# Optimization experiments

Measured on AMD Instinct MI355X. Metric: run time of the kernel, lower is better.

## Reference

```python
import jax, jax.numpy as jnp
import numpy as np

N_HEAD = 16

def setup_inputs() -> dict:
    key = jax.random.key(0)
    k1, k2, k3 = jax.random.split(key, 3)
    B, S, D = 2, 2048, 1024
    x = jax.random.normal(k1, (B, S, D), dtype=jnp.float32)
    w_attn = jax.random.normal(k2, (D, 3 * D), dtype=jnp.float32) * 0.02
    b_attn = jnp.zeros((3 * D,), dtype=jnp.float32)
    w_proj = jax.random.normal(k3, (D, D), dtype=jnp.float32) * 0.02
    b_proj = jnp.zeros((D,), dtype=jnp.float32)
    return {"x": x, "w_attn": w_attn, "b_attn": b_attn, "w_proj": w_proj, "b_proj": b_proj}

def reference(x, w_attn, b_attn, w_proj, b_proj):
    B, S, D = x.shape
    hd = D // N_HEAD
    qkv = x @ w_attn + b_attn                      # [B,S,3D]
    q, k, v = jnp.split(qkv, 3, axis=-1)
    def heads(t):  # [B,S,D] -> [B,H,S,hd]
        return t.reshape(B, S, N_HEAD, hd).transpose(0, 2, 1, 3)
    q, k, v = heads(q), heads(k), heads(v)
    # NOTE: original forward applies NO scaling and NO causal mask; dropout=eval (identity)
    scores = jnp.einsum('bhqd,bhkd->bhqk', q, k)   # [B,H,S,S]
    probs = jax.nn.softmax(scores, axis=-1)
    out = jnp.einsum('bhqk,bhkd->bhqd', probs, v)  # [B,H,S,hd]
    out = out.transpose(0, 2, 1, 3).reshape(B, S, D)
    return out @ w_proj + b_proj
```

## Files before the change

kernel.cpp:

```cpp
#include <hip/hip_runtime.h>

typedef _Float16 f16;
typedef _Float16 f16x8 __attribute__((ext_vector_type(8)));
typedef _Float16 f16x4 __attribute__((ext_vector_type(4)));
typedef float    f32x4 __attribute__((ext_vector_type(4)));
typedef unsigned int u32;
typedef unsigned int u32x4 __attribute__((ext_vector_type(4)));

#define LOG2E 1.44269504088896340736f
#define EXPC  (13.0f * 1.44269504088896340736f)

__device__ __forceinline__ void gload_lds16(const void* g, void* l) {
  __builtin_amdgcn_global_load_lds(
      (const __attribute__((address_space(1))) void*)g,
      (__attribute__((address_space(3))) void*)l, 16, 0, 0);
}

__device__ __forceinline__ void block_sync() {
  asm volatile("" ::: "memory");
  __builtin_amdgcn_s_barrier();
  asm volatile("" ::: "memory");
}

__global__ __launch_bounds__(256)
void k_prep(const float* __restrict__ x, f16* __restrict__ xh,
            const float* __restrict__ w_attn, f16* __restrict__ waT,
            const float* __restrict__ w_proj, f16* __restrict__ wpT) {
  __shared__ float tile[32][33];
  const int bid = blockIdx.x;
  const int t = threadIdx.x;
  if (bid < 4096) {
    int i = bid * 256 + t;
    f32x4 v = ((const f32x4*)x)[i];
    f16x4 o;
    o[0] = (f16)v[0]; o[1] = (f16)v[1]; o[2] = (f16)v[2]; o[3] = (f16)v[3];
    ((f16x4*)xh)[i] = o;
    return;
  }
  const float* in; f16* out; int R, C, bx, by;
  if (bid < 4096 + 3072) {
    int q = bid - 4096; in = w_attn; out = waT; R = 1024; C = 3072;
    bx = q % 96; by = q / 96;
  } else {
    int q = bid - 7168; in = w_proj; out = wpT; R = 1024; C = 1024;
    bx = q % 32; by = q / 32;
  }
  int tx = t & 31, ty = t >> 5;
  int c0 = bx * 32, r0 = by * 32;
#pragma unroll
  for (int i = 0; i < 4; i++)
    tile[ty + i * 8][tx] = in[(size_t)(r0 + ty + i * 8) * C + c0 + tx];
  __syncthreads();
#pragma unroll
  for (int i = 0; i < 4; i++)
    out[(size_t)(c0 + ty + i * 8) * R + r0 + tx] = (f16)tile[tx][ty + i * 8];
}

template <int EPI>
__global__ __launch_bounds__(256)
void k_gemm(const f16* __restrict__ A, const f16* __restrict__ BT,
            const float* __restrict__ bias,
            f16* __restrict__ out_qk, f16* __restrict__ out_vT,
            float* __restrict__ out_f) {
  constexpr int K = 1024;
  __shared__ f16 smem[4][128 * 64];
  const int t = threadIdx.x;
  const int l = t & 63;
  const int w = t >> 6;
  const int wm = (w >> 1) * 64;
  const int wn = (w & 1) * 64;
  const int m0 = blockIdx.x * 128;
  const int n0 = blockIdx.y * 128;
  const int lr = l & 15;
  const int lg = l >> 4;
  const int fr8 = lr & 7;

  const int row8g = t >> 3;
  const int scg = (t & 7) ^ (row8g & 7);
  const f16* Ap = A + (size_t)(m0 + row8g) * K + scg * 8;
  const f16* Bp = BT + (size_t)(n0 + row8g) * K + scg * 8;

#define GSTAGE(buf) do { \
    _Pragma("unroll") \
    for (int i2 = 0; i2 < 4; i2++) \
      gload_lds16(Ap + (size_t)(i2 * 32) * K, &smem[buf][(i2 * 256 + t) * 8]); \
    _Pragma("unroll") \
    for (int i2 = 0; i2 < 4; i2++) \
      gload_lds16(Bp + (size_t)(i2 * 32) * K, &smem[2 + buf][(i2 * 256 + t) * 8]); \
    Ap += 64; Bp += 64; } while (0)

  f32x4 acc[4][4] = {};

#define GCOMPUTE(buf) do { \
    _Pragma("unroll") \
    for (int kk = 0; kk < 64; kk += 32) { \
      const int cbase = (kk >> 3) + lg; \
      f16x8 af[4], bf[4]; \
      _Pragma("unroll") \
      for (int i = 0; i < 4; i++) \
        af[i] = *(const f16x8*)&smem[buf][((wm + i * 16 + lr) * 8 + (cbase ^ fr8)) * 8]; \
      _Pragma("unroll") \
      for (int j = 0; j < 4; j++) \
        bf[j] = *(const f16x8*)&smem[2 + buf][((wn + j * 16 + lr) * 8 + (cbase ^ fr8)) * 8]; \
      _Pragma("unroll") \
      for (int i = 0; i < 4; i++) \
        _Pragma("unroll") \
        for (int j = 0; j < 4; j++) \
          acc[i][j] = __builtin_amdgcn_mfma_f32_16x16x32_f16(af[i], bf[j], acc[i][j], 0, 0, 0); \
    } } while (0)

  GSTAGE(0);
  asm volatile("s_waitcnt vmcnt(0)" ::: "memory");
  block_sync();

  for (int kt = 0; kt < 16; kt += 2) {
    GSTAGE(1);
    GCOMPUTE(0);
    asm volatile("s_waitcnt vmcnt(0)" ::: "memory");
    block_sync();
    if (kt + 2 < 16) GSTAGE(0);
    GCOMPUTE(1);
    asm volatile("s_waitcnt vmcnt(0)" ::: "memory");
    block_sync();
  }
#undef GSTAGE
#undef GCOMPUTE

  if (EPI == 1) {
#pragma unroll
    for (int i = 0; i < 4; i++) {
      int mbase = m0 + wm + i * 16 + (l >> 4) * 4;
#pragma unroll
      for (int j = 0; j < 4; j++) {
        int n = n0 + wn + j * 16 + lr;
        float bv = bias[n];
#pragma unroll
        for (int r = 0; r < 4; r++)
          out_f[(size_t)(mbase + r) * 1024 + n] = acc[i][j][r] + bv;
      }
    }
  } else if (n0 < 2048) {
#pragma unroll
    for (int i = 0; i < 4; i++) {
      int mbase = m0 + wm + i * 16 + (l >> 4) * 4;
#pragma unroll
      for (int j = 0; j < 4; j++) {
        int n = n0 + wn + j * 16 + lr;
        float bv = bias[n];
        float sc = (n0 + wn + j * 16 < 1024) ? LOG2E : 1.0f;
#pragma unroll
        for (int r = 0; r < 4; r++)
          out_qk[(size_t)(mbase + r) * 2048 + n] = (f16)((acc[i][j][r] + bv) * sc);
      }
    }
  } else {
    f16* scr = &smem[0][0];
#pragma unroll
    for (int i = 0; i < 4; i++) {
      int s0 = wm + i * 16 + (l >> 4) * 4;
#pragma unroll
      for (int j = 0; j < 4; j++) {
        int nl = wn + j * 16 + lr;
        float bv = bias[n0 + nl];
        f16x4 pv;
#pragma unroll
        for (int r = 0; r < 4; r++) pv[r] = (f16)(acc[i][j][r] + bv);
        *(f16x4*)&scr[nl * 128 + (s0 ^ ((nl & 15) << 3))] = pv;
      }
    }
    block_sync();
    const int b = m0 >> 11;
    const int kvc0 = (m0 & 2047) >> 3;
    const int h0 = (n0 - 2048) >> 6;
    const int l64 = t & 63;
    const int wv = t >> 6;
#pragma unroll
    for (int p = 0; p < 8; p++) {
      int pair = wv + p * 4;
      int kvcl = pair & 15;
      int hgl  = pair >> 4;
      int nl = hgl * 64 + l64;
      f16x8 vv = *(const f16x8*)&scr[nl * 128 + ((kvcl * 8) ^ ((nl & 15) << 3))];
      size_t dst = (((size_t)(b * 16 + h0 + hgl) * 256 + kvc0 + kvcl) * 64 + l64) * 8;
      *(f16x8*)&out_vT[dst] = vv;
    }
  }
}

__global__ __launch_bounds__(256, 4)
void k_attn(const f16* __restrict__ qk, const f16* __restrict__ vT,
            f16* __restrict__ aout) {
  __shared__ f16 Kl[2][64 * 64];
  const int t = threadIdx.x;
  const int l = t & 63;
  const int w = t >> 6;
  const int lr = l & 15;
  const int lg = l >> 4;
  const int lk = lg * 8;
  const int r7x = lr & 7;

  const int o  = (blockIdx.x & 7) * 128 + (blockIdx.x >> 3);
  const int qt = o & 31;
  const int bh = o >> 5;
  const int b  = bh >> 4;
  const int h  = bh & 15;
  const int q0 = qt * 64 + w * 16;

  const f16* qp = qk + (size_t)(b * 2048 + q0 + lr) * 2048 + h * 64 + lk;
  f16x8 qf0 = *(const f16x8*)qp;
  f16x8 qf1 = *(const f16x8*)(qp + 32);

  const f16* kg = qk + (size_t)(b * 2048) * 2048 + 1024 + h * 64;
  const int r5 = t >> 3;
  const int u_s = r5 & 15;
  const int prow = (u_s >> 2) * 8 + (u_s & 3) * 2 + (r5 >> 4);
  const int sc_s = ((t & 7) ^ (r5 & 7)) << 3;

  const f16* vg0 = vT + (((size_t)bh * 256 + lg) * 64 + lr) * 8;

#define STAGE(B) do { \
    gload_lds16(kg + (size_t)(prow     ) * 2048 + sc_s, &Kl[B][(      t) * 8]); \
    gload_lds16(kg + (size_t)(prow + 32) * 2048 + sc_s, &Kl[B][(256 + t) * 8]); \
    kg += 64 * 2048; } while (0)

  f32x4 oa[4] = {};
  f32x4 ssum = {};
  const f32x4 initc = {-EXPC, -EXPC, -EXPC, -EXPC};
  f16x8 ones;
#pragma unroll
  for (int j = 0; j < 8; j++) ones[j] = (f16)1.0f;

  STAGE(0);
  asm volatile("s_waitcnt vmcnt(0)" ::: "memory");
  block_sync();

#define TILE_BODY(B) do { \
    f16x8 vfr[4][2]; \
    _Pragma("unroll") \
    for (int c4 = 0; c4 < 4; c4++) \
      _Pragma("unroll") \
      for (int ks = 0; ks < 2; ks++) \
        vfr[c4][ks] = *(const f16x8*)(vg0 + ks * 2048 + c4 * 128); \
    f32x4 sa[4]; \
    __builtin_amdgcn_s_setprio(1); \
    _Pragma("unroll") \
    for (int c = 0; c < 4; c++) { \
      const int ks = c >> 1, cc = c & 1; \
      const int row = ks * 32 + cc * 16 + lr; \
      f16x8 kf0 = *(const f16x8*)&Kl[B][(row * 8 + (lg ^ r7x)) * 8]; \
      f16x8 kf1 = *(const f16x8*)&Kl[B][(row * 8 + ((lg + 4) ^ r7x)) * 8]; \
      sa[c] = __builtin_amdgcn_mfma_f32_16x16x32_f16(kf0, qf0, initc, 0, 0, 0); \
      sa[c] = __builtin_amdgcn_mfma_f32_16x16x32_f16(kf1, qf1, sa[c], 0, 0, 0); \
    } \
    __builtin_amdgcn_s_setprio(0); \
    _Pragma("unroll") \
    for (int c = 0; c < 4; c++) \
      _Pragma("unroll") \
      for (int r = 0; r < 4; r++) \
        sa[c][r] = __builtin_amdgcn_exp2f(sa[c][r]); \
    u32 pka[2][4]; \
    _Pragma("unroll") \
    for (int ks = 0; ks < 2; ks++) \
      _Pragma("unroll") \
      for (int u = 0; u < 4; u++) \
        pka[ks][u] = __builtin_bit_cast(u32, \
            __builtin_amdgcn_cvt_pkrtz(sa[2 * ks][u], sa[2 * ks + 1][u])); \
    f16x8 pa0 = __builtin_bit_cast(f16x8, (u32x4){pka[0][0], pka[0][1], pka[0][2], pka[0][3]}); \
    f16x8 pa1 = __builtin_bit_cast(f16x8, (u32x4){pka[1][0], pka[1][1], pka[1][2], pka[1][3]}); \
    __builtin_amdgcn_s_setprio(1); \
    ssum = __builtin_amdgcn_mfma_f32_16x16x32_f16(pa0, ones, ssum, 0, 0, 0); \
    ssum = __builtin_amdgcn_mfma_f32_16x16x32_f16(pa1, ones, ssum, 0, 0, 0); \
    _Pragma("unroll") \
    for (int c4 = 0; c4 < 4; c4++) { \
      oa[c4] = __builtin_amdgcn_mfma_f32_16x16x32_f16(pa0, vfr[c4][0], oa[c4], 0, 0, 0); \
      oa[c4] = __builtin_amdgcn_mfma_f32_16x16x32_f16(pa1, vfr[c4][1], oa[c4], 0, 0, 0); \
    } \
    __builtin_amdgcn_s_setprio(0); \
    vg0 += 4096; \
    asm volatile("s_waitcnt vmcnt(0)" ::: "memory"); \
    block_sync(); } while (0)

  for (int tt = 0; tt < 32; tt += 2) {
    STAGE(1);
    TILE_BODY(0);
    if (tt + 2 < 32) STAGE(0);
    TILE_BODY(1);
  }
#undef STAGE
#undef TILE_BODY

#pragma unroll
  for (int r = 0; r < 4; r++) {
    float ia = 1.0f / ssum[r];
    size_t rowa = (size_t)(b * 2048 + q0 + lg * 4 + r);
#pragma unroll
    for (int c4 = 0; c4 < 4; c4++)
      aout[rowa * 1024 + h * 64 + c4 * 16 + lr] = (f16)(oa[c4][r] * ia);
  }
}

extern "C" void kernel_launch(void* const* d_in, const int* in_sizes, int n_in,
                              void* d_out, int out_size, void* d_ws, size_t ws_size,
                              hipStream_t stream) {
  const float* x      = (const float*)d_in[0];
  const float* w_attn = (const float*)d_in[1];
  const float* b_attn = (const float*)d_in[2];
  const float* w_proj = (const float*)d_in[3];
  const float* b_proj = (const float*)d_in[4];
  float* out = (float*)d_out;

  char* p = (char*)d_ws;
  f16* xh  = (f16*)p;  p += (size_t)4096 * 1024 * 2;
  f16* waT = (f16*)p;  p += (size_t)3072 * 1024 * 2;
  f16* wpT = (f16*)p;  p += (size_t)1024 * 1024 * 2;
  f16* qkb = (f16*)p;  p += (size_t)4096 * 2048 * 2;
  f16* vTb = (f16*)p;  p += (size_t)32 * 256 * 64 * 8 * 2;
  f16* aob = (f16*)p;  p += (size_t)4096 * 1024 * 2;
  if ((size_t)(p - (char*)d_ws) > ws_size) return;

  k_prep<<<8192, 256, 0, stream>>>(x, xh, w_attn, waT, w_proj, wpT);
  k_gemm<0><<<dim3(32, 24), 256, 0, stream>>>(xh, waT, b_attn, qkb, vTb, nullptr);
  k_attn<<<1024, 256, 0, stream>>>(qkb, vTb, aob);
  k_gemm<1><<<dim3(32, 8), 256, 0, stream>>>(aob, wpT, b_proj, nullptr, nullptr, out);
}
```

Before: 111.6 us.

## Quad-buffer K tiles and process two KV tiles per barrier

Grows the shared K buffer from two stages to four. Each loop iteration now waits once, loads V fragments for two KV tiles, prefetches the next two K tiles, and then computes both tiles. This halves the number of vmcnt waits and block barriers in the attention loop and gives loads more time to land. In exchange it uses twice the LDS per block and holds V fragments for two tiles in registers at once, which raises register pressure under the 4-blocks-per-CU launch bound and could cause spills.

```diff
diff --git a/kernel.cpp b/kernel.cpp
--- a/kernel.cpp
+++ b/kernel.cpp
@@ -190,7 +190,7 @@
 __global__ __launch_bounds__(256, 4)
 void k_attn(const f16* __restrict__ qk, const f16* __restrict__ vT,
             f16* __restrict__ aout) {
-  __shared__ f16 Kl[2][64 * 64];
+  __shared__ f16 Kl[4][64 * 64];
   const int t = threadIdx.x;
   const int l = t & 63;
   const int w = t >> 6;
@@ -230,17 +230,7 @@
 #pragma unroll
   for (int j = 0; j < 8; j++) ones[j] = (f16)1.0f;
 
-  STAGE(0);
-  asm volatile("s_waitcnt vmcnt(0)" ::: "memory");
-  block_sync();
-
-#define TILE_BODY(B) do { \
-    f16x8 vfr[4][2]; \
-    _Pragma("unroll") \
-    for (int c4 = 0; c4 < 4; c4++) \
-      _Pragma("unroll") \
-      for (int ks = 0; ks < 2; ks++) \
-        vfr[c4][ks] = *(const f16x8*)(vg0 + ks * 2048 + c4 * 128); \
+#define TILE_BODY(B, VFR) do { \
     f32x4 sa[4]; \
     __builtin_amdgcn_s_setprio(1); \
     _Pragma("unroll") \
@@ -272,19 +262,37 @@
     ssum = __builtin_amdgcn_mfma_f32_16x16x32_f16(pa1, ones, ssum, 0, 0, 0); \
     _Pragma("unroll") \
     for (int c4 = 0; c4 < 4; c4++) { \
-      oa[c4] = __builtin_amdgcn_mfma_f32_16x16x32_f16(pa0, vfr[c4][0], oa[c4], 0, 0, 0); \
-      oa[c4] = __builtin_amdgcn_mfma_f32_16x16x32_f16(pa1, vfr[c4][1], oa[c4], 0, 0, 0); \
+      oa[c4] = __builtin_amdgcn_mfma_f32_16x16x32_f16(pa0, VFR[c4][0], oa[c4], 0, 0, 0); \
+      oa[c4] = __builtin_amdgcn_mfma_f32_16x16x32_f16(pa1, VFR[c4][1], oa[c4], 0, 0, 0); \
     } \
-    __builtin_amdgcn_s_setprio(0); \
-    vg0 += 4096; \
-    asm volatile("s_waitcnt vmcnt(0)" ::: "memory"); \
-    block_sync(); } while (0)
-
-  for (int tt = 0; tt < 32; tt += 2) {
-    STAGE(1);
-    TILE_BODY(0);
-    if (tt + 2 < 32) STAGE(0);
-    TILE_BODY(1);
+    __builtin_amdgcn_s_setprio(0); } while (0)
+
+  STAGE(0);
+  STAGE(1);
+
+  for (int p = 0; p < 16; ++p) {
+    asm volatile("s_waitcnt vmcnt(0)" ::: "memory");
+    block_sync();
+
+    f16x8 vfrA[4][2], vfrB[4][2];
+#pragma unroll
+    for (int c4 = 0; c4 < 4; c4++)
+#pragma unroll
+      for (int ks = 0; ks < 2; ks++) {
+        vfrA[c4][ks] = *(const f16x8*)(vg0 + ks * 2048 + c4 * 128);
+        vfrB[c4][ks] = *(const f16x8*)(vg0 + 4096 + ks * 2048 + c4 * 128);
+      }
+    vg0 += 8192;
+
+    const int cb = (p & 1) << 1;
+    const int nb = ((p + 1) & 1) << 1;
+    if (p < 15) {
+      STAGE(nb);
+      STAGE(nb + 1);
+    }
+
+    TILE_BODY(cb, vfrA);
+    TILE_BODY(cb + 1, vfrB);
   }
 #undef STAGE
 #undef TILE_BODY
```

Result: slower. 147.3 us (+32.0%).
